# Optimization experiments

Hardware: AMD Instinct MI355X
Metric: run time of the kernel (lower is better)

The kernel has to match this reference:

```python
import jax, jax.numpy as jnp
from jax import lax
import numpy as np

MAX_SEQ_LEN = 8192
B, S, D = 8, 8192, 1024
LN_EPS = 1e-5

# ---------- static lattice structure (pure Python, replicates original incl. quirks) ----------

def _gen_spine(max_len):
    s = [0, 2, 4]
    while True:
        nxt = 2 * s[-1] + 2 * s[-2] + 2 * s[-3]
        if nxt >= max_len:
            break
        s.append(nxt)
    return s

def _imm_anc(spine, pos):
    if pos in spine:
        i = spine.index(pos)
        if i >= 3:
            return [spine[i - 1], spine[i - 2], spine[i - 3]]
    return []

def _analyze(spine, pos):
    # BFS over ancestors; NOTE: levels[level+1] is OVERWRITTEN per popped node,
    # exactly as in the original torch code.
    visited = {pos}
    levels = {0: [pos]}
    queue = [(pos, 0)]
    while queue:
        cur, lvl = queue.pop(0)
        if lvl >= 9:
            break
        newl = []
        for a in _imm_anc(spine, cur):
            if a not in visited and a >= 0:
                visited.add(a)
                newl.append(a)
                queue.append((a, lvl + 1))
        if newl:
            levels[lvl + 1] = list(newl)
    max_depth = max(levels.keys())
    pc = {pos: 1}
    for lvl in sorted(levels.keys(), reverse=True):
        for node in levels[lvl]:
            if node == pos:
                continue
            if lvl == max_depth:
                pc[node] = 1
                continue
            c = 0
            for ch in levels.get(lvl + 1, []):
                if node in _imm_anc(spine, ch):
                    c += pc.get(ch, 0)
            if lvl != 0:
                pc[node] = c
    pc.pop(pos, None)
    return levels, pc

def _structures(seq_len):
    spine = _gen_spine(MAX_SEQ_LEN)
    out = []
    for pos in spine:
        if pos >= seq_len or pos < 3:
            continue
        levels, pc = _analyze(spine, pos)
        anc, cnt = [], []
        for lvl in levels:  # dict insertion order == level order, as in torch
            if lvl > 0:
                for a in levels[lvl]:
                    if a < seq_len:
                        anc.append(a)
                        cnt.append(float(pc.get(a, 1)))
        if anc:
            out.append((pos, np.array(anc, np.int32), np.array(cnt, np.float32)))
    return out

# ---------- neural pieces ----------

def _gru_last(seq, w_ih, w_hh, b_ih, b_hh):
    # seq: [B, K, D]; single-layer batch_first GRU, h0 = 0; returns last hidden [B, D]
    d = w_hh.shape[1]
    def step(h, xt):
        gi = xt @ w_ih.T + b_ih   # [B, 3D]
        gh = h @ w_hh.T + b_hh
        i_r, i_z, i_n = jnp.split(gi, 3, axis=-1)
        h_r, h_z, h_n = jnp.split(gh, 3, axis=-1)
        r = jax.nn.sigmoid(i_r + h_r)
        z = jax.nn.sigmoid(i_z + h_z)
        n = jnp.tanh(i_n + r * h_n)
        return (1.0 - z) * n + z * h, None
    h0 = jnp.zeros((seq.shape[0], d), seq.dtype)
    hT, _ = lax.scan(step, h0, jnp.swapaxes(seq, 0, 1))
    return hT

def reference(x, pw_w1, pw_b1, pw_w2, pw_b2, msg_w, msg_b, ln_g, ln_b,
              gru_w_ih, gru_w_hh, gru_b_ih, gru_b_hh, gate_w, gate_b):
    structs = _structures(x.shape[1])
    out = x
    for pos, anc, cnt in structs:
        # path weights: Linear(1,64)->ReLU->Linear(64,1)->Softplus  on counts [K,1]
        c = jnp.asarray(cnt)[:, None]
        w = jax.nn.softplus(jnp.squeeze(jax.nn.relu(c @ pw_w1.T + pw_b1) @ pw_w2.T + pw_b2))  # [K]
        h_anc = x[:, anc, :]                         # [B, K, D] gather
        h_cur = x[:, pos, :]                         # [B, D]
        pair = jnp.concatenate([h_anc, jnp.broadcast_to(h_cur[:, None, :], h_anc.shape)], axis=-1)
        m = pair @ msg_w.T + msg_b                   # [B, K, D]
        mu = m.mean(-1, keepdims=True)
        var = ((m - mu) ** 2).mean(-1, keepdims=True)
        m = (m - mu) / jnp.sqrt(var + LN_EPS) * ln_g + ln_b
        m = jax.nn.gelu(m, approximate=False)
        m = m * w[None, :, None]                     # path-weighted messages
        agg = _gru_last(m, gru_w_ih, gru_w_hh, gru_b_ih, gru_b_hh)  # [B, D]
        g = jax.nn.sigmoid(jnp.concatenate([agg, h_cur], axis=-1) @ gate_w.T + gate_b)
        out = out.at[:, pos, :].set(g * agg + (1.0 - g) * h_cur)
    return out

def setup_inputs() -> dict:
    key = jax.random.key(0)
    ks = jax.random.split(key, 8)
    def n(k, shape, s=0.02):
        return jax.random.normal(k, shape, jnp.float32) * s
    return {
        "x": jax.random.normal(ks[0], (B, S, D), jnp.float32),
        "pw_w1": n(ks[1], (64, 1), 0.5), "pw_b1": jnp.zeros((64,), jnp.float32),
        "pw_w2": n(ks[2], (1, 64), 0.5), "pw_b2": jnp.zeros((1,), jnp.float32),
        "msg_w": n(ks[3], (D, 2 * D)), "msg_b": jnp.zeros((D,), jnp.float32),
        "ln_g": jnp.ones((D,), jnp.float32), "ln_b": jnp.zeros((D,), jnp.float32),
        "gru_w_ih": n(ks[4], (3 * D, D)), "gru_w_hh": n(ks[5], (3 * D, D)),
        "gru_b_ih": jnp.zeros((3 * D,), jnp.float32), "gru_b_hh": jnp.zeros((3 * D,), jnp.float32),
        "gate_w": n(ks[6], (D, 2 * D)), "gate_b": jnp.zeros((D,), jnp.float32),
    }
```

## Files before the change

### kernel.cpp

```cpp
#include <hip/hip_runtime.h>
#include <math.h>

#define SEQ 8192
#define DIM 1024
#define NBATCH 8

typedef float vf4 __attribute__((ext_vector_type(4)));

struct SDesc {
  int n, Tmax, totalRows;
  int pos[8], A[8], rowbase[8];
  int anc[8][8];
  float cnt[8][8];
  int nu;
  int upos[16];
  int up_of_s[8];
  int s_of_rr[32], a_of_rr[32], ua_of_rr[32];
};

static SDesc build_structs() {
  SDesc H{};
  int spine[24];
  int ns = 3; spine[0] = 0; spine[1] = 2; spine[2] = 4;
  for (;;) {
    long nxt = 2L * (spine[ns-1] + spine[ns-2] + spine[ns-3]);
    if (nxt >= SEQ) break;
    spine[ns++] = (int)nxt;
  }
  int rb = 0;
  for (int i = 0; i < ns; ++i) {
    int pos = spine[i];
    if (pos < 3) continue;
    bool visited[24] = {false};
    int levels[12][8]; int lcnt[12];
    for (int l = 0; l < 12; ++l) lcnt[l] = 0;
    levels[0][0] = i; lcnt[0] = 1; visited[i] = true;
    int qidx[64], qlvl[64], qh = 0, qt = 0;
    qidx[qt] = i; qlvl[qt] = 0; qt++;
    int maxd = 0;
    while (qh < qt) {
      int cur = qidx[qh], lvl = qlvl[qh]; qh++;
      if (lvl >= 9) break;
      int newl[8], nn = 0;
      if (cur >= 3) {
        for (int d = 1; d <= 3; ++d) {
          int a = cur - d;
          if (!visited[a]) { visited[a] = true; newl[nn++] = a; qidx[qt] = a; qlvl[qt] = lvl + 1; qt++; }
        }
      }
      if (nn) {
        lcnt[lvl+1] = nn;
        for (int k = 0; k < nn; ++k) levels[lvl+1][k] = newl[k];
        if (lvl + 1 > maxd) maxd = lvl + 1;
      }
    }
    float pcv[24]; bool pcs[24];
    for (int k = 0; k < 24; ++k) { pcv[k] = 0.f; pcs[k] = false; }
    pcv[i] = 1.f; pcs[i] = true;
    for (int lvl = maxd; lvl >= 0; --lvl) {
      for (int nidx = 0; nidx < lcnt[lvl]; ++nidx) {
        int node = levels[lvl][nidx];
        if (node == i) continue;
        if (lvl == maxd) { pcv[node] = 1.f; pcs[node] = true; continue; }
        float c = 0.f;
        for (int cidx = 0; cidx < lcnt[lvl+1]; ++cidx) {
          int ch = levels[lvl+1][cidx];
          if (ch >= 3 && node >= ch - 3 && node <= ch - 1) c += pcs[ch] ? pcv[ch] : 0.f;
        }
        if (lvl != 0) { pcv[node] = c; pcs[node] = true; }
      }
    }
    int A = 0;
    int sidx = H.n;
    for (int lvl = 1; lvl <= maxd; ++lvl) {
      for (int nidx = 0; nidx < lcnt[lvl]; ++nidx) {
        int node = levels[lvl][nidx];
        H.anc[sidx][A] = spine[node];
        H.cnt[sidx][A] = pcs[node] ? pcv[node] : 1.f;
        A++;
      }
    }
    if (A == 0) continue;
    H.pos[sidx] = pos; H.A[sidx] = A; H.rowbase[sidx] = rb; rb += A;
    H.n++;
  }
  H.totalRows = rb;
  H.Tmax = 0;
  for (int s = 0; s < H.n; ++s) if (H.A[s] > H.Tmax) H.Tmax = H.A[s];
  int vals[128], nv = 0;
  for (int s = 0; s < H.n; ++s) {
    vals[nv++] = H.pos[s];
    for (int a = 0; a < H.A[s]; ++a) vals[nv++] = H.anc[s][a];
  }
  H.nu = 0;
  for (int i = 0; i < nv; ++i) {
    bool seen = false;
    for (int u = 0; u < H.nu; ++u) if (H.upos[u] == vals[i]) { seen = true; break; }
    if (!seen) H.upos[H.nu++] = vals[i];
  }
  for (int i = 0; i < H.nu; ++i)
    for (int j2 = i + 1; j2 < H.nu; ++j2)
      if (H.upos[j2] < H.upos[i]) { int t = H.upos[i]; H.upos[i] = H.upos[j2]; H.upos[j2] = t; }
  auto uidx = [&](int v) { for (int u = 0; u < H.nu; ++u) if (H.upos[u] == v) return u; return 0; };
  for (int s = 0; s < H.n; ++s) {
    H.up_of_s[s] = uidx(H.pos[s]);
    for (int a = 0; a < H.A[s]; ++a) {
      int rr = H.rowbase[s] + a;
      H.s_of_rr[rr] = s; H.a_of_rr[rr] = a; H.ua_of_rr[rr] = uidx(H.anc[s][a]);
    }
  }
  return H;
}


__device__ __forceinline__ float wred(float v) {
  #pragma unroll
  for (int off = 32; off; off >>= 1) v += __shfl_xor(v, off);
  return v;
}

__device__ __forceinline__ float dot4(vf4 a, vf4 b) {
  return a.x * b.x + a.y * b.y + a.z * b.z + a.w * b.w;
}

__device__ __forceinline__ void do_copy(const vf4* __restrict__ src, vf4* __restrict__ dst,
                                        int q, int nc, int start4, int n4) {
  for (int i = q * 256 + threadIdx.x; i < n4; i += nc * 256) {
    vf4 v = __builtin_nontemporal_load(&src[start4 + i]);
    __builtin_nontemporal_store(v, &dst[start4 + i]);
  }
}

__global__ __launch_bounds__(256, 4) void k_T(SDesc sd, const float* __restrict__ x,
    const float* __restrict__ msg_w, float* __restrict__ T,
    const float* __restrict__ w1, const float* __restrict__ b1,
    const float* __restrict__ w2, const float* __restrict__ b2, float* __restrict__ wout,
    const vf4* __restrict__ csrc, vf4* __restrict__ cdst, int cstart, int cn) {
  int p = blockIdx.x;
  const int NMAIN = 1280;
  if (p > NMAIN) { do_copy(csrc, cdst, p - NMAIN - 1, 2048, cstart, cn); return; }
  if (p == NMAIN) {
    int t = threadIdx.x;
    int s = t >> 3, a = t & 7;
    if (t < 64 && s < sd.n && a < sd.A[s]) {
      float v = sd.cnt[s][a];
      float acc = 0.f;
      for (int i = 0; i < 64; ++i) {
        float h = v * w1[i] + b1[i];
        if (h > 0.f) acc += h * w2[i];
      }
      float o = acc + b2[0];
      wout[s * 8 + a] = (o > 0.f) ? (o + log1pf(expf(-o))) : log1pf(expf(o));
    }
    return;
  }
  int q = p % 128, rt = p / 128;
  int jt = (q & 7) * 16 + (q >> 3);
  int wave = threadIdx.x >> 6, lane = threadIdx.x & 63;
  int jc0 = jt * 16 + wave * 4;
  const vf4* mw4 = (const vf4*)msg_w;
  size_t wb0 = (size_t)((jc0 + 0) & 1023) * 512 + ((size_t)((jc0 + 0) >> 10) << 8);
  size_t wb1 = (size_t)((jc0 + 1) & 1023) * 512 + ((size_t)((jc0 + 1) >> 10) << 8);
  size_t wb2 = (size_t)((jc0 + 2) & 1023) * 512 + ((size_t)((jc0 + 2) >> 10) << 8);
  size_t wb3 = (size_t)((jc0 + 3) & 1023) * 512 + ((size_t)((jc0 + 3) >> 10) << 8);
  vf4 tw0[4], tw1[4], tw2[4], tw3[4];
  #pragma unroll
  for (int c = 0; c < 4; ++c) {
    tw0[c] = mw4[wb0 + c * 64 + lane];
    tw1[c] = mw4[wb1 + c * 64 + lane];
    tw2[c] = mw4[wb2 + c * 64 + lane];
    tw3[c] = mw4[wb3 + c * 64 + lane];
  }
  const vf4* x4 = (const vf4*)x;
  #pragma unroll 2
  for (int r = 0; r < 8; ++r) {
    int row = rt * 8 + r; int uq = row >> 3, bb = row & 7;
    size_t rb4 = ((size_t)bb * SEQ + sd.upos[uq]) * 256;
    vf4 a0 = x4[rb4 + 0 * 64 + lane], a1 = x4[rb4 + 1 * 64 + lane];
    vf4 a2 = x4[rb4 + 2 * 64 + lane], a3 = x4[rb4 + 3 * 64 + lane];
    float s0 = dot4(tw0[0], a0) + dot4(tw0[1], a1) + dot4(tw0[2], a2) + dot4(tw0[3], a3);
    float s1 = dot4(tw1[0], a0) + dot4(tw1[1], a1) + dot4(tw1[2], a2) + dot4(tw1[3], a3);
    float s2 = dot4(tw2[0], a0) + dot4(tw2[1], a1) + dot4(tw2[2], a2) + dot4(tw2[3], a3);
    float s3 = dot4(tw3[0], a0) + dot4(tw3[1], a1) + dot4(tw3[2], a2) + dot4(tw3[3], a3);
    s0 = wred(s0); s1 = wred(s1); s2 = wred(s2); s3 = wred(s3);
    if (lane == 0) {
      float* tp = T + (size_t)row * 2048 + jc0;
      tp[0] = s0; tp[1] = s1; tp[2] = s2; tp[3] = s3;
    }
  }
}

__global__ __launch_bounds__(256) void k_ln(SDesc sd, const float* __restrict__ ln_g,
    const float* __restrict__ ln_b, const float* __restrict__ msg_b,
    const float* __restrict__ wsc, const float* __restrict__ T, float* __restrict__ mseq,
    const vf4* __restrict__ csrc, vf4* __restrict__ cdst, int cstart, int cn) {
  int p = blockIdx.x;
  if (p >= 240) { do_copy(csrc, cdst, p - 240, 2048, cstart, cn); return; }
  int rr = p >> 3, bb = p & 7;
  int s = sd.s_of_rr[rr], aa = sd.a_of_rr[rr];
  int ua = sd.ua_of_rr[rr], up = sd.up_of_s[s];
  float wmul = wsc[s * 8 + aa];
  const vf4* Tl = (const vf4*)(T + ((size_t)ua * 8 + bb) * 2048);
  const vf4* Tr = (const vf4*)(T + ((size_t)up * 8 + bb) * 2048 + 1024);
  const vf4* mb = (const vf4*)msg_b;
  int t = threadIdx.x;
  vf4 vl = Tl[t], vr = Tr[t], vb = mb[t];
  vf4 v; v.x = vl.x + vr.x + vb.x; v.y = vl.y + vr.y + vb.y;
  v.z = vl.z + vr.z + vb.z; v.w = vl.w + vr.w + vb.w;
  float sum = v.x + v.y + v.z + v.w;
  float sq  = v.x * v.x + v.y * v.y + v.z * v.z + v.w * v.w;
  #pragma unroll
  for (int off = 32; off; off >>= 1) { sum += __shfl_xor(sum, off); sq += __shfl_xor(sq, off); }
  __shared__ float s1m[4], s2m[4];
  int wave = t >> 6, lane = t & 63;
  if (lane == 0) { s1m[wave] = sum; s2m[wave] = sq; }
  __syncthreads();
  sum = s1m[0] + s1m[1] + s1m[2] + s1m[3];
  sq  = s2m[0] + s2m[1] + s2m[2] + s2m[3];
  float mu  = sum * (1.f / 1024.f);
  float var = sq * (1.f / 1024.f) - mu * mu;
  float inv = rsqrtf(var + 1e-5f);
  vf4 g4 = ((const vf4*)ln_g)[t];
  vf4 b4 = ((const vf4*)ln_b)[t];
  float o[4]  = {v.x, v.y, v.z, v.w};
  float gg[4] = {g4.x, g4.y, g4.z, g4.w};
  float bb2[4] = {b4.x, b4.y, b4.z, b4.w};
  #pragma unroll
  for (int i = 0; i < 4; ++i) {
    float u = (o[i] - mu) * inv * gg[i] + bb2[i];
    float ge = 0.5f * u * (1.f + erff(u * 0.70710678118654752f));
    o[i] = ge * wmul;
  }
  vf4 ov; ov.x = o[0]; ov.y = o[1]; ov.z = o[2]; ov.w = o[3];
  ((vf4*)(mseq + (size_t)p * DIM))[t] = ov;
}

__global__ __launch_bounds__(256, 4) void k_gi(SDesc sd, const float* __restrict__ mseq,
    const float* __restrict__ wih, const float* __restrict__ bih,
    const float* __restrict__ bhh, float* __restrict__ gi, float* __restrict__ h1,
    const vf4* __restrict__ csrc, vf4* __restrict__ cdst, int cstart, int cn) {
  int p = blockIdx.x;
  const int NMAIN = 1280;
  if (p >= NMAIN) { do_copy(csrc, cdst, p - NMAIN, 2048, cstart, cn); return; }
  int q = p % 256, rt = p / 256;
  int jt = (q & 7) * 32 + (q >> 3);
  int wave = threadIdx.x >> 6, lane = threadIdx.x & 63;
  int j = jt * 4 + wave;

  const vf4* wp4 = (const vf4*)wih;
  vf4 wr[4], wz[4], wn[4];
  #pragma unroll
  for (int c = 0; c < 4; ++c) {
    wr[c] = wp4[(size_t)j * 256 + c * 64 + lane];
    wz[c] = wp4[(size_t)(1024 + j) * 256 + c * 64 + lane];
    wn[c] = wp4[(size_t)(2048 + j) * 256 + c * 64 + lane];
  }
  float bi_r = bih[j], bi_z = bih[1024 + j], bi_n = bih[2048 + j];
  float bh_r = bhh[j], bh_z = bhh[1024 + j], bh_n = bhh[2048 + j];

  __shared__ float lrow[8][1024];
  int rowbase = rt * 48;
  for (int ch = 0; ch < 6; ++ch) {
    __syncthreads();
    for (int idx = threadIdx.x; idx < 8 * 256; idx += 256) {
      int r = idx >> 8, c = idx & 255;
      ((vf4*)lrow[r])[c] = ((const vf4*)(mseq + (size_t)(rowbase + ch * 8 + r) * DIM))[c];
    }
    __syncthreads();
    for (int r = 0; r < 8; ++r) {
      int row = rowbase + ch * 8 + r;
      const vf4* hp = (const vf4*)lrow[r];
      vf4 a0 = hp[0 * 64 + lane], a1 = hp[1 * 64 + lane];
      vf4 a2 = hp[2 * 64 + lane], a3 = hp[3 * 64 + lane];
      float sr = dot4(wr[0], a0) + dot4(wr[1], a1) + dot4(wr[2], a2) + dot4(wr[3], a3);
      float sz = dot4(wz[0], a0) + dot4(wz[1], a1) + dot4(wz[2], a2) + dot4(wz[3], a3);
      float sn = dot4(wn[0], a0) + dot4(wn[1], a1) + dot4(wn[2], a2) + dot4(wn[3], a3);
      sr = wred(sr); sz = wred(sz); sn = wred(sn);
      if (lane == 0) {
        sr += bi_r; sz += bi_z; sn += bi_n;
        float* gp = gi + (size_t)row * 3072;
        gp[j] = sr; gp[1024 + j] = sz; gp[2048 + j] = sn;
        int rr = row >> 3;
        int s = sd.s_of_rr[rr];
        if (sd.a_of_rr[rr] == 0 && sd.A[s] == sd.Tmax) {
          float rg = 1.f / (1.f + expf(-(sr + bh_r)));
          float zg = 1.f / (1.f + expf(-(sz + bh_z)));
          float ng = tanhf(sn + rg * bh_n);
          h1[(size_t)(s * 8 + (row & 7)) * DIM + j] = (1.f - zg) * ng;
        }
      }
    }
  }
}

__global__ __launch_bounds__(256, 4) void k_step(SDesc sd, int t,
    const float* __restrict__ whh, const float* __restrict__ bhh,
    const float* __restrict__ gi, const float* __restrict__ hold, float* __restrict__ hnew,
    const vf4* __restrict__ csrc, vf4* __restrict__ cdst, int cstart, int cn) {
  int p = blockIdx.x;
  const int NMAIN = 7 * 256;
  if (p >= NMAIN) { do_copy(csrc, cdst, p - NMAIN, 1536, cstart, cn); return; }
  int q = p & 255, s = p >> 8;
  int jt = (q & 7) * 32 + (q >> 3);
  int t0 = sd.Tmax - sd.A[s];
  if (t < t0) return;
  int a = t - t0;

  int wave = threadIdx.x >> 6, lane = threadIdx.x & 63;
  int j = jt * 4 + wave;
  int girow0 = (sd.rowbase[s] + a) * 8;

  if (a == 0) {
    if (lane < 8) {
      int r = lane;
      const float* gp = gi + (size_t)(girow0 + r) * 3072;
      float rg = 1.f / (1.f + expf(-(gp[j] + bhh[j])));
      float zg = 1.f / (1.f + expf(-(gp[1024 + j] + bhh[1024 + j])));
      float ng = tanhf(gp[2048 + j] + rg * bhh[2048 + j]);
      hnew[(size_t)(s * 8 + r) * DIM + j] = (1.f - zg) * ng;
    }
    return;
  }

  const vf4* wp4 = (const vf4*)whh;
  vf4 wr[4], wz[4], wn[4];
  #pragma unroll
  for (int c = 0; c < 4; ++c) {
    wr[c] = wp4[(size_t)j * 256 + c * 64 + lane];
    wz[c] = wp4[(size_t)(1024 + j) * 256 + c * 64 + lane];
    wn[c] = wp4[(size_t)(2048 + j) * 256 + c * 64 + lane];
  }
  float bj_r = bhh[j], bj_z = bhh[1024 + j], bj_n = bhh[2048 + j];
  const vf4* h4 = (const vf4*)hold;
  #pragma unroll 2
  for (int r = 0; r < 8; ++r) {
    int srow = s * 8 + r;
    size_t rb4 = (size_t)srow * 256;
    const float* gp = gi + (size_t)(girow0 + r) * 3072;
    float gir = gp[j], giz = gp[1024 + j], gin = gp[2048 + j];
    vf4 a0 = h4[rb4 + 0 * 64 + lane], a1 = h4[rb4 + 1 * 64 + lane];
    vf4 a2 = h4[rb4 + 2 * 64 + lane], a3 = h4[rb4 + 3 * 64 + lane];
    float ar = dot4(wr[0], a0) + dot4(wr[1], a1) + dot4(wr[2], a2) + dot4(wr[3], a3);
    float az = dot4(wz[0], a0) + dot4(wz[1], a1) + dot4(wz[2], a2) + dot4(wz[3], a3);
    float an = dot4(wn[0], a0) + dot4(wn[1], a1) + dot4(wn[2], a2) + dot4(wn[3], a3);
    ar = wred(ar); az = wred(az); an = wred(an);
    if (lane == 0) {
      float rg = 1.f / (1.f + expf(-(gir + ar + bj_r)));
      float zg = 1.f / (1.f + expf(-(giz + az + bj_z)));
      float ng = tanhf(gin + rg * (an + bj_n));
      float ho = hold[(size_t)srow * DIM + j];
      hnew[(size_t)srow * DIM + j] = (1.f - zg) * ng + zg * ho;
    }
  }
}

__global__ __launch_bounds__(256, 4) void k_gate(SDesc sd, const float* __restrict__ x,
    const float* __restrict__ gw, const float* __restrict__ gb,
    const float* __restrict__ hfin, float* __restrict__ out) {
  int p = blockIdx.x;
  int q = p % 128, rt = p / 128;
  int jt = (q & 7) * 16 + (q >> 3);

  int wave = threadIdx.x >> 6, lane = threadIdx.x & 63;
  int j0 = jt * 8 + wave * 2;
  const vf4* g4p = (const vf4*)gw;
  vf4 wL0[4], wR0[4], wL1[4], wR1[4];
  #pragma unroll
  for (int c = 0; c < 4; ++c) {
    wL0[c] = g4p[(size_t)(j0 + 0) * 512 + c * 64 + lane];
    wR0[c] = g4p[(size_t)(j0 + 0) * 512 + 256 + c * 64 + lane];
    wL1[c] = g4p[(size_t)(j0 + 1) * 512 + c * 64 + lane];
    wR1[c] = g4p[(size_t)(j0 + 1) * 512 + 256 + c * 64 + lane];
  }
  const vf4* h4 = (const vf4*)hfin;
  const vf4* x4 = (const vf4*)x;
  #pragma unroll 2
  for (int r = 0; r < 8; ++r) {
    int row = rt * 8 + r; int s = row >> 3, bb = row & 7;
    size_t ab4 = (size_t)row * 256;
    size_t xb4 = ((size_t)bb * SEQ + sd.pos[s]) * 256;
    vf4 a0 = h4[ab4 + 0 * 64 + lane], a1 = h4[ab4 + 1 * 64 + lane];
    vf4 a2 = h4[ab4 + 2 * 64 + lane], a3 = h4[ab4 + 3 * 64 + lane];
    vf4 x0 = x4[xb4 + 0 * 64 + lane], x1 = x4[xb4 + 1 * 64 + lane];
    vf4 x2 = x4[xb4 + 2 * 64 + lane], x3 = x4[xb4 + 3 * 64 + lane];
    float s0 = dot4(wL0[0], a0) + dot4(wL0[1], a1) + dot4(wL0[2], a2) + dot4(wL0[3], a3)
             + dot4(wR0[0], x0) + dot4(wR0[1], x1) + dot4(wR0[2], x2) + dot4(wR0[3], x3);
    float s1 = dot4(wL1[0], a0) + dot4(wL1[1], a1) + dot4(wL1[2], a2) + dot4(wL1[3], a3)
             + dot4(wR1[0], x0) + dot4(wR1[1], x1) + dot4(wR1[2], x2) + dot4(wR1[3], x3);
    s0 = wred(s0); s1 = wred(s1);
    if (lane == 0) {
      #pragma unroll
      for (int jj = 0; jj < 2; ++jj) {
        int j = j0 + jj;
        float sv = jj ? s1 : s0;
        float g = 1.f / (1.f + expf(-(sv + gb[j])));
        float agg = hfin[(size_t)row * DIM + j];
        float hc  = x[((size_t)bb * SEQ + sd.pos[s]) * DIM + j];
        out[((size_t)bb * SEQ + sd.pos[s]) * DIM + j] = g * agg + (1.f - g) * hc;
      }
    }
  }
}


extern "C" void kernel_launch(void* const* d_in, const int* in_sizes, int n_in,
                              void* d_out, int out_size, void* d_ws, size_t ws_size,
                              hipStream_t stream) {
  const float* x      = (const float*)d_in[0];
  const float* pw_w1  = (const float*)d_in[1];
  const float* pw_b1  = (const float*)d_in[2];
  const float* pw_w2  = (const float*)d_in[3];
  const float* pw_b2  = (const float*)d_in[4];
  const float* msg_w  = (const float*)d_in[5];
  const float* msg_b  = (const float*)d_in[6];
  const float* ln_g   = (const float*)d_in[7];
  const float* ln_b   = (const float*)d_in[8];
  const float* w_ih   = (const float*)d_in[9];
  const float* w_hh   = (const float*)d_in[10];
  const float* b_ih   = (const float*)d_in[11];
  const float* b_hh   = (const float*)d_in[12];
  const float* gate_w = (const float*)d_in[13];
  const float* gate_b = (const float*)d_in[14];
  float* out = (float*)d_out;
  float* ws  = (float*)d_ws;

  SDesc sd = build_structs();

  float* wout = ws;
  float* T    = wout + 64;
  float* mseq = T + (size_t)sd.nu * 8 * 2048;
  float* gi   = mseq + (size_t)240 * DIM;
  float* h0   = gi + (size_t)240 * 3072;
  float* h1   = h0 + (size_t)sd.n * 8 * DIM;

  const vf4* x4 = (const vf4*)x;
  vf4* out4 = (vf4*)out;
  const int TOTAL4 = (NBATCH * SEQ * DIM) / 4;
  const int c_big = 3300000;
  const int rem = TOTAL4 - 3 * c_big;
  const int c_s = rem / 4;

  int off = 0;
  k_T<<<1281 + 2048, 256, 0, stream>>>(sd, x, msg_w, T, pw_w1, pw_b1, pw_w2, pw_b2, wout,
                                       x4, out4, off, c_big);
  off += c_big;

  k_ln<<<240 + 2048, 256, 0, stream>>>(sd, ln_g, ln_b, msg_b, wout, T, mseq,
                                       x4, out4, off, c_big);
  off += c_big;

  k_gi<<<1280 + 2048, 256, 0, stream>>>(sd, mseq, w_ih, b_ih, b_hh, gi, h1,
                                        x4, out4, off, c_big);
  off += c_big;

  for (int t = 1; t <= 4; ++t) {
    const float* hr = (t & 1) ? h1 : h0;
    float*       hw = (t & 1) ? h0 : h1;
    int cnt = (t == 4) ? (TOTAL4 - off) : c_s;
    k_step<<<1792 + 1536, 256, 0, stream>>>(sd, t, w_hh, b_hh, gi, hr, hw,
                                            x4, out4, off, cnt);
    off += cnt;
  }
  k_gate<<<896, 256, 0, stream>>>(sd, x, gate_w, gate_b, h1, out);

  (void)in_sizes; (void)n_in; (void)out_size; (void)ws_size;
}
```

Baseline: 276.7 us.

## Rebalance x-to-out copy across first three kernels and drop it from GRU steps

The bulk copy of x into out, previously spread across the first three kernels and the four recurrent step kernels, now goes entirely to the first three kernels in equal thirds. Copy blocks are put at the front of each grid and their count is raised to 3072. The step kernels no longer carry copy work, which shortens the serial recurrent chain. The cost is longer front kernels, and the main compute blocks may now be scheduled after the copy blocks instead of alongside them.

```diff
diff --git a/kernel.cpp b/kernel.cpp
--- a/kernel.cpp
+++ b/kernel.cpp
@@ -131,15 +131,17 @@
   }
 }
 
+#define NC 3072
+
 __global__ __launch_bounds__(256, 4) void k_T(SDesc sd, const float* __restrict__ x,
     const float* __restrict__ msg_w, float* __restrict__ T,
     const float* __restrict__ w1, const float* __restrict__ b1,
     const float* __restrict__ w2, const float* __restrict__ b2, float* __restrict__ wout,
     const vf4* __restrict__ csrc, vf4* __restrict__ cdst, int cstart, int cn) {
   int p = blockIdx.x;
-  const int NMAIN = 1280;
-  if (p > NMAIN) { do_copy(csrc, cdst, p - NMAIN - 1, 2048, cstart, cn); return; }
-  if (p == NMAIN) {
+  if (p < NC) { do_copy(csrc, cdst, p, NC, cstart, cn); return; }
+  int pm = p - NC;
+  if (pm == 1280) {
     int t = threadIdx.x;
     int s = t >> 3, a = t & 7;
     if (t < 64 && s < sd.n && a < sd.A[s]) {
@@ -154,7 +156,7 @@
     }
     return;
   }
-  int q = p % 128, rt = p / 128;
+  int q = pm % 128, rt = pm / 128;
   int jt = (q & 7) * 16 + (q >> 3);
   int wave = threadIdx.x >> 6, lane = threadIdx.x & 63;
   int jc0 = jt * 16 + wave * 4;
@@ -190,13 +192,14 @@
   }
 }
 
-__global__ __launch_bounds__(256) void k_ln(SDesc sd, const float* __restrict__ ln_g,
+__global__ __launch_bounds__(256, 4) void k_ln(SDesc sd, const float* __restrict__ ln_g,
     const float* __restrict__ ln_b, const float* __restrict__ msg_b,
     const float* __restrict__ wsc, const float* __restrict__ T, float* __restrict__ mseq,
     const vf4* __restrict__ csrc, vf4* __restrict__ cdst, int cstart, int cn) {
   int p = blockIdx.x;
-  if (p >= 240) { do_copy(csrc, cdst, p - 240, 2048, cstart, cn); return; }
-  int rr = p >> 3, bb = p & 7;
+  if (p < NC) { do_copy(csrc, cdst, p, NC, cstart, cn); return; }
+  int pm = p - NC;
+  int rr = pm >> 3, bb = pm & 7;
   int s = sd.s_of_rr[rr], aa = sd.a_of_rr[rr];
   int ua = sd.ua_of_rr[rr], up = sd.up_of_s[s];
   float wmul = wsc[s * 8 + aa];
@@ -232,7 +235,7 @@
     o[i] = ge * wmul;
   }
   vf4 ov; ov.x = o[0]; ov.y = o[1]; ov.z = o[2]; ov.w = o[3];
-  ((vf4*)(mseq + (size_t)p * DIM))[t] = ov;
+  ((vf4*)(mseq + (size_t)pm * DIM))[t] = ov;
 }
 
 __global__ __launch_bounds__(256, 4) void k_gi(SDesc sd, const float* __restrict__ mseq,
@@ -240,9 +243,9 @@
     const float* __restrict__ bhh, float* __restrict__ gi, float* __restrict__ h1,
     const vf4* __restrict__ csrc, vf4* __restrict__ cdst, int cstart, int cn) {
   int p = blockIdx.x;
-  const int NMAIN = 1280;
-  if (p >= NMAIN) { do_copy(csrc, cdst, p - NMAIN, 2048, cstart, cn); return; }
-  int q = p % 256, rt = p / 256;
+  if (p < NC) { do_copy(csrc, cdst, p, NC, cstart, cn); return; }
+  int pm = p - NC;
+  int q = pm % 256, rt = pm / 256;
   int jt = (q & 7) * 32 + (q >> 3);
   int wave = threadIdx.x >> 6, lane = threadIdx.x & 63;
   int j = jt * 4 + wave;
@@ -295,11 +298,8 @@
 
 __global__ __launch_bounds__(256, 4) void k_step(SDesc sd, int t,
     const float* __restrict__ whh, const float* __restrict__ bhh,
-    const float* __restrict__ gi, const float* __restrict__ hold, float* __restrict__ hnew,
-    const vf4* __restrict__ csrc, vf4* __restrict__ cdst, int cstart, int cn) {
+    const float* __restrict__ gi, const float* __restrict__ hold, float* __restrict__ hnew) {
   int p = blockIdx.x;
-  const int NMAIN = 7 * 256;
-  if (p >= NMAIN) { do_copy(csrc, cdst, p - NMAIN, 1536, cstart, cn); return; }
   int q = p & 255, s = p >> 8;
   int jt = (q & 7) * 32 + (q >> 3);
   int t0 = sd.Tmax - sd.A[s];
@@ -436,30 +436,23 @@
   const vf4* x4 = (const vf4*)x;
   vf4* out4 = (vf4*)out;
   const int TOTAL4 = (NBATCH * SEQ * DIM) / 4;
-  const int c_big = 3300000;
-  const int rem = TOTAL4 - 3 * c_big;
-  const int c_s = rem / 4;
-
-  int off = 0;
-  k_T<<<1281 + 2048, 256, 0, stream>>>(sd, x, msg_w, T, pw_w1, pw_b1, pw_w2, pw_b2, wout,
-                                       x4, out4, off, c_big);
-  off += c_big;
-
-  k_ln<<<240 + 2048, 256, 0, stream>>>(sd, ln_g, ln_b, msg_b, wout, T, mseq,
-                                       x4, out4, off, c_big);
-  off += c_big;
-
-  k_gi<<<1280 + 2048, 256, 0, stream>>>(sd, mseq, w_ih, b_ih, b_hh, gi, h1,
-                                        x4, out4, off, c_big);
-  off += c_big;
+  const int c1 = TOTAL4 / 3;
+  const int c2 = c1;
+  const int c3 = TOTAL4 - c1 - c2;
+
+  k_T<<<NC + 1281, 256, 0, stream>>>(sd, x, msg_w, T, pw_w1, pw_b1, pw_w2, pw_b2, wout,
+                                     x4, out4, 0, c1);
+
+  k_ln<<<NC + 240, 256, 0, stream>>>(sd, ln_g, ln_b, msg_b, wout, T, mseq,
+                                     x4, out4, c1, c2);
+
+  k_gi<<<NC + 1280, 256, 0, stream>>>(sd, mseq, w_ih, b_ih, b_hh, gi, h1,
+                                      x4, out4, c1 + c2, c3);
 
   for (int t = 1; t <= 4; ++t) {
     const float* hr = (t & 1) ? h1 : h0;
     float*       hw = (t & 1) ? h0 : h1;
-    int cnt = (t == 4) ? (TOTAL4 - off) : c_s;
-    k_step<<<1792 + 1536, 256, 0, stream>>>(sd, t, w_hh, b_hh, gi, hr, hw,
-                                            x4, out4, off, cnt);
-    off += cnt;
+    k_step<<<1792, 256, 0, stream>>>(sd, t, w_hh, b_hh, gi, hr, hw);
   }
   k_gate<<<896, 256, 0, stream>>>(sd, x, gate_w, gate_b, h1, out);
 
```

New measurement: 295.5 us. +6.8%, slower.
